# Optimization experiments

Hardware: AMD Instinct MI355X
Metric: run time of the kernel (lower is better)

## Reference

```python
import jax, jax.numpy as jnp
import numpy as np
import math

D_MODEL = 512
N_HEADS = 8
D_K = D_MODEL // N_HEADS
N_SAMPLES = 16
BETA = 1.0
SCALE = 1.0 / math.sqrt(D_K)
PROPOSAL_TEMP = 0.5


def setup_inputs() -> dict:
    key = jax.random.key(0)
    ks = jax.random.split(key, 9)
    B, S = 2, 512
    x = jax.random.normal(ks[0], (B, S, D_MODEL), dtype=jnp.float32)
    init = lambda k: jax.random.normal(k, (D_MODEL, D_MODEL), dtype=jnp.float32) * 0.02
    return {
        "x": x,
        "Wq": init(ks[1]), "bq": jnp.zeros((D_MODEL,), jnp.float32),
        "Wk": init(ks[2]), "bk": jnp.zeros((D_MODEL,), jnp.float32),
        "Wv": init(ks[3]), "bv": jnp.zeros((D_MODEL,), jnp.float32),
        "Wo": init(ks[4]), "bo": jnp.zeros((D_MODEL,), jnp.float32),
    }


def _importance_sampled_weights(scores):
    # scores: [B,H,S,S]. Replicates the per-row Python loop, fully vectorized.
    B, H, Sq, Sk = scores.shape
    target = jax.nn.softmax(scores * BETA, axis=-1)            # [B,H,Sq,Sk]
    # optimal proposal: 0.5*target + 0.5*uniform
    prop = PROPOSAL_TEMP * target + (1.0 - PROPOSAL_TEMP) / Sk
    R = B * H * Sq
    tf = target.reshape(R, Sk)
    pf = prop.reshape(R, Sk)
    # tsu_backend.sample_binary_layer(log(p/(1-p))) == Bernoulli(p) sampling
    s = jax.random.bernoulli(jax.random.key(42), pf[:, None, :], (R, N_SAMPLES, Sk))
    # importance weight = prod(target[sel]) / (prod(prop[sel]) * prod(1-prop[~sel]))
    pt = jnp.prod(jnp.where(s, tf[:, None, :], 1.0), axis=-1)                 # [R,N]
    pp = jnp.prod(jnp.where(s, pf[:, None, :], 1.0 - pf[:, None, :]), axis=-1)
    valid = (s.sum(-1) > 0) & (pp > 0)
    w = jnp.where(valid, pt / jnp.maximum(pp, 1e-38), 0.0)
    ws = w.sum(-1, keepdims=True)
    w = jnp.where(ws > 0, w / jnp.maximum(ws, 1e-38), 1.0 / N_SAMPLES)        # [R,N]
    wa = jnp.einsum('rn,rnk->rk', w, s.astype(jnp.float32))                   # [R,Sk]
    was = wa.sum(-1, keepdims=True)
    wa = jnp.where(was > 0, wa / jnp.maximum(was, 1e-38), 1.0 / Sk)
    return wa.reshape(B, H, Sq, Sk)


def reference(x, Wq, bq, Wk, bk, Wv, bv, Wo, bo):
    B, S, Dm = x.shape
    proj = lambda W, b: (x @ W + b).reshape(B, S, N_HEADS, D_K).transpose(0, 2, 1, 3)
    Q = proj(Wq, bq)  # [B,H,S,dk]
    K = proj(Wk, bk)
    V = proj(Wv, bv)
    scores = jnp.einsum('bhqd,bhkd->bhqk', Q, K) * SCALE
    # torch builds weights via torch.tensor(...) which detaches => constant w.r.t. params
    attn = jax.lax.stop_gradient(_importance_sampled_weights(scores))
    out = jnp.einsum('bhqk,bhkd->bhqd', attn, V)
    out = out.transpose(0, 2, 1, 3).reshape(B, S, Dm)
    return out @ Wo + bo
```

## Files before the change

### kernel.cpp

```cpp
#include <hip/hip_runtime.h>
#include <cstdint>
#include <cstddef>


#define ROTL(x, r) __builtin_rotateleft32((x), (r))

#define QR8(s)                                                                \
  x0[0]+=x1[0];x0[1]+=x1[1];x0[2]+=x1[2];x0[3]+=x1[3];                        \
  x0[4]+=x1[4];x0[5]+=x1[5];x0[6]+=x1[6];x0[7]+=x1[7];                        \
  x1[0]=ROTL(x1[0],s);x1[1]=ROTL(x1[1],s);x1[2]=ROTL(x1[2],s);                \
  x1[3]=ROTL(x1[3],s);x1[4]=ROTL(x1[4],s);x1[5]=ROTL(x1[5],s);                \
  x1[6]=ROTL(x1[6],s);x1[7]=ROTL(x1[7],s);                                    \
  x1[0]^=x0[0];x1[1]^=x0[1];x1[2]^=x0[2];x1[3]^=x0[3];                        \
  x1[4]^=x0[4];x1[5]^=x0[5];x1[6]^=x0[6];x1[7]^=x0[7];
#define INJ8(X, Y)                                                            \
  x0[0]+=(X);x0[1]+=(X);x0[2]+=(X);x0[3]+=(X);                                \
  x0[4]+=(X);x0[5]+=(X);x0[6]+=(X);x0[7]+=(X);                                \
  x1[0]+=(Y);x1[1]+=(Y);x1[2]+=(Y);x1[3]+=(Y);                                \
  x1[4]+=(Y);x1[5]+=(Y);x1[6]+=(Y);x1[7]+=(Y);
#define INJ8Y(Y)                                                              \
  x1[0]+=(Y);x1[1]+=(Y);x1[2]+=(Y);x1[3]+=(Y);                                \
  x1[4]+=(Y);x1[5]+=(Y);x1[6]+=(Y);x1[7]+=(Y);

__global__ __launch_bounds__(256)
void qkv_gemm(const float* __restrict__ x,
              const float* __restrict__ Wq, const float* __restrict__ bq,
              const float* __restrict__ Wk, const float* __restrict__ bk,
              const float* __restrict__ Wv, const float* __restrict__ bv,
              const float* __restrict__ bo, float* __restrict__ outp,
              float* __restrict__ Qw, float* __restrict__ KTw,
              float* __restrict__ Vw) {
  const int tid = threadIdx.x;
  if (blockIdx.z == 3) {
    const int blk = blockIdx.y * 16 + blockIdx.x;
    const size_t base4 = (size_t)blk * 1024 + tid;
    const float4* bo4 = (const float4*)bo;
    float4* out4 = (float4*)outp;
#pragma unroll
    for (int i = 0; i < 4; ++i) {
      const size_t idx4 = base4 + (size_t)i * 256;
      out4[idx4] = bo4[idx4 & 127];
    }
    return;
  }
  const float* W; const float* bias;
  if (blockIdx.z == 0)      { W = Wq; bias = bq; }
  else if (blockIdx.z == 1) { W = Wk; bias = bk; }
  else                      { W = Wv; bias = bv; }

  __shared__ __align__(16) float smem[64 * 68];
  float (*At)[68] = (float(*)[68])smem;
  float (*Bs)[64] = (float(*)[64])(smem + 32 * 68);
  float (*T2)[68] = (float(*)[68])smem;

  const int tx = tid & 15, ty = tid >> 4;
  const int row0 = blockIdx.x * 64, col0 = blockIdx.y * 64;
  float acc[4][4] = {};

  for (int kk = 0; kk < 512; kk += 32) {
    const int ar = tid >> 2;
#pragma unroll
    for (int i = 0; i < 2; ++i) {
      const int kc = ((tid & 3) << 3) + (i << 2);
      const float4 a4 =
          *(const float4*)&x[(size_t)(row0 + ar) * 512 + kk + kc];
      At[kc + 0][ar] = a4.x; At[kc + 1][ar] = a4.y;
      At[kc + 2][ar] = a4.z; At[kc + 3][ar] = a4.w;
    }
#pragma unroll
    for (int i = 0; i < 2; ++i) {
      const int idx = tid + (i << 8);
      const int br = idx >> 4, bc = (idx & 15) << 2;
      *(float4*)&Bs[br][bc] =
          *(const float4*)&W[(size_t)(kk + br) * 512 + col0 + bc];
    }
    __syncthreads();
#pragma unroll
    for (int p = 0; p < 32; ++p) {
      const float4 a4 = *(const float4*)&At[p][ty << 2];
      const float4 b4 = *(const float4*)&Bs[p][tx << 2];
      acc[0][0] = fmaf(a4.x, b4.x, acc[0][0]); acc[0][1] = fmaf(a4.x, b4.y, acc[0][1]);
      acc[0][2] = fmaf(a4.x, b4.z, acc[0][2]); acc[0][3] = fmaf(a4.x, b4.w, acc[0][3]);
      acc[1][0] = fmaf(a4.y, b4.x, acc[1][0]); acc[1][1] = fmaf(a4.y, b4.y, acc[1][1]);
      acc[1][2] = fmaf(a4.y, b4.z, acc[1][2]); acc[1][3] = fmaf(a4.y, b4.w, acc[1][3]);
      acc[2][0] = fmaf(a4.z, b4.x, acc[2][0]); acc[2][1] = fmaf(a4.z, b4.y, acc[2][1]);
      acc[2][2] = fmaf(a4.z, b4.z, acc[2][2]); acc[2][3] = fmaf(a4.z, b4.w, acc[2][3]);
      acc[3][0] = fmaf(a4.w, b4.x, acc[3][0]); acc[3][1] = fmaf(a4.w, b4.y, acc[3][1]);
      acc[3][2] = fmaf(a4.w, b4.z, acc[3][2]); acc[3][3] = fmaf(a4.w, b4.w, acc[3][3]);
    }
    __syncthreads();
  }

  if (blockIdx.z == 0) {
#pragma unroll
    for (int i = 0; i < 4; ++i) {
      const int row = row0 + (ty << 2) + i;
      const int b = row >> 9, s = row & 511;
#pragma unroll
      for (int j = 0; j < 4; ++j) {
        const int col = col0 + (tx << 2) + j;
        const int h = col >> 6, d = col & 63;
        Qw[(((size_t)(b * 8 + h) * 512 + s) * 64) + d] = acc[i][j] + bias[col];
      }
    }
  } else if (blockIdx.z == 1) {
#pragma unroll
    for (int i = 0; i < 4; ++i) {
#pragma unroll
      for (int j = 0; j < 4; ++j) {
        const int col = col0 + (tx << 2) + j;
        T2[(tx << 2) + j][(ty << 2) + i] = acc[i][j] + bias[col];
      }
    }
    __syncthreads();
    const int c = tid >> 2, seg = tid & 3;
    const int b = row0 >> 9, h = blockIdx.y;
    const int s0 = (row0 & 511) + (seg << 4);
    float* dst = KTw + (((size_t)(b * 8 + h) * 64 + c) << 9) + s0;
#pragma unroll
    for (int i2 = 0; i2 < 4; ++i2) {
      *(float4*)&dst[i2 << 2] = *(const float4*)&T2[c][(seg << 4) + (i2 << 2)];
    }
  } else {
#pragma unroll
    for (int i = 0; i < 4; ++i) {
      const int row = row0 + (ty << 2) + i;
      const int b = row >> 9, s = row & 511;
#pragma unroll
      for (int j = 0; j < 4; ++j) {
        const int col = col0 + (tx << 2) + j;
        const int h = col >> 6, d = col & 63;
        Vw[(((size_t)(b * 8 + h) * 512 + s) * 64) + d] = acc[i][j] + bias[col];
      }
    }
  }
}

__global__ __launch_bounds__(256)
void fused_sample(const float* __restrict__ Q, const float* __restrict__ KT,
                  const float* __restrict__ V, const float* __restrict__ Wo,
                  float* __restrict__ outp) {
  const int r = ((blockIdx.x & 7) << 10) + (blockIdx.x >> 3);
  const int bh = r >> 9, q = r & 511;
  const int b = r >> 12, h = (r >> 9) & 7;
  const int tid = threadIdx.x;
  __shared__ __align__(16) float qs[64];
  __shared__ float red[8];
  __shared__ float tf[512];
  __shared__ __align__(16) uint32_t pscu2[512];
  __shared__ float wa[512];
  __shared__ float wr[16];
  __shared__ float redc[8];
  __shared__ float psum[4][64];
  __shared__ float o_s[64];
  __shared__ int   list[512];
  __shared__ int   cnt;

  if (tid == 0) cnt = 0;
  if (tid < 64) qs[tid] = Q[((size_t)bh * 512 + q) * 64 + tid];
  __syncthreads();

  float sc[2];
#pragma unroll
  for (int ii = 0; ii < 2; ++ii) {
    const int k = tid + (ii << 8);
    const float* Kp = KT + (size_t)bh * 64 * 512 + k;
    float s = 0.f;
#pragma unroll
    for (int d4 = 0; d4 < 16; ++d4) {
      const float4 qv = ((const float4*)qs)[d4];
      const float k0 = Kp[(size_t)(d4 * 4 + 0) * 512];
      const float k1 = Kp[(size_t)(d4 * 4 + 1) * 512];
      const float k2 = Kp[(size_t)(d4 * 4 + 2) * 512];
      const float k3 = Kp[(size_t)(d4 * 4 + 3) * 512];
      s = fmaf(qv.x, k0, s); s = fmaf(qv.y, k1, s);
      s = fmaf(qv.z, k2, s); s = fmaf(qv.w, k3, s);
    }
    sc[ii] = s * 0.125f;
  }
  float mx = fmaxf(sc[0], sc[1]);
  for (int m = 1; m < 64; m <<= 1) mx = fmaxf(mx, __shfl_xor(mx, m));
  if ((tid & 63) == 0) red[tid >> 6] = mx;
  __syncthreads();
  const float rowmax = fmaxf(fmaxf(red[0], red[1]), fmaxf(red[2], red[3]));
  const float e0 = expf(sc[0] - rowmax);
  const float e1 = expf(sc[1] - rowmax);
  float ssum = e0 + e1;
  for (int m = 1; m < 64; m <<= 1) ssum += __shfl_xor(ssum, m);
  if ((tid & 63) == 0) red[4 + (tid >> 6)] = ssum;
  __syncthreads();
  const float tot = red[4] + red[5] + red[6] + red[7];
  const float t0 = e0 / tot, t1 = e1 / tot;
  tf[tid] = t0; tf[tid + 256] = t1;
  wa[tid] = 0.f; wa[tid + 256] = 0.f;
  {
    const float p0 = fmaf(0.5f, t0, 0.0009765625f);
    const float p1 = fmaf(0.5f, t1, 0.0009765625f);
    {
      const int k = tid;
      pscu2[(((k & 31) >> 2) << 6) + ((k >> 5) << 2) + (k & 3)] =
          ((uint32_t)ceilf(p0 * 8388608.0f)) << 9;
    }
    {
      const int k = tid + 256;
      pscu2[(((k & 31) >> 2) << 6) + ((k >> 5) << 2) + (k & 3)] =
          ((uint32_t)ceilf(p1 * 8388608.0f)) << 9;
    }
    float ql = (1.f - p0) * (1.f - p1);
    for (int m = 1; m < 64; m <<= 1) ql *= __shfl_xor(ql, m);
    if ((tid & 63) == 0) redc[4 + (tid >> 6)] = ql;
  }
  __syncthreads();
  const float Qrow = redc[4] * redc[5] * redc[6] * redc[7];

  const int n = tid >> 4, t = tid & 15;
  const int k0i = t << 5;
  const uint32_t cbase =
      (uint32_t)r * 8192u + (uint32_t)n * 512u + (uint32_t)k0i + 42u;
  uint32_t bits = 0u;
#pragma unroll
  for (int jb = 0; jb < 32; jb += 8) {
    uint32_t x0[8], x1[8];
#pragma unroll
    for (int i = 0; i < 8; ++i) {
      const uint32_t c = cbase + (uint32_t)(jb + i);
      x0[i] = c;
      x1[i] = ROTL(c, 13) ^ c;
    }
    QR8(15) QR8(26) QR8(6)
    INJ8(42u, 0x1BD11BF1u)
    QR8(17) QR8(29) QR8(16) QR8(24)
    INJ8(0x1BD11BF0u, 2u)
    QR8(13) QR8(15) QR8(26) QR8(6)
    INJ8Y(45u)
    QR8(17) QR8(29) QR8(16) QR8(24)
    INJ8(42u, 0x1BD11BF4u)
    QR8(13) QR8(15) QR8(26) QR8(6)
    INJ8(0x1BD11BF0u, 5u)
    const uint4 pA = *(const uint4*)&pscu2[((jb >> 2) << 6) + (t << 2)];
    const uint4 pB = *(const uint4*)&pscu2[(((jb >> 2) + 1) << 6) + (t << 2)];
    bits |= (uint32_t)((x0[0] ^ x1[0]) < pA.x) << (jb + 0);
    bits |= (uint32_t)((x0[1] ^ x1[1]) < pA.y) << (jb + 1);
    bits |= (uint32_t)((x0[2] ^ x1[2]) < pA.z) << (jb + 2);
    bits |= (uint32_t)((x0[3] ^ x1[3]) < pA.w) << (jb + 3);
    bits |= (uint32_t)((x0[4] ^ x1[4]) < pB.x) << (jb + 4);
    bits |= (uint32_t)((x0[5] ^ x1[5]) < pB.y) << (jb + 5);
    bits |= (uint32_t)((x0[6] ^ x1[6]) < pB.z) << (jb + 6);
    bits |= (uint32_t)((x0[7] ^ x1[7]) < pB.w) << (jb + 7);
  }

  float ptl = 1.f, ratl = 1.f;
  int cl = __popc(bits);
  {
    uint32_t bb = bits;
    while (bb) {
      const int j = __builtin_ctz(bb);
      bb &= bb - 1u;
      const float tv = tf[k0i + j];
      const float p = fmaf(0.5f, tv, 0.0009765625f);
      ptl *= tv;
      ratl *= p / (1.f - p);
    }
  }
#pragma unroll
  for (int m = 1; m < 16; m <<= 1) {
    ptl *= __shfl_xor(ptl, m);
    ratl *= __shfl_xor(ratl, m);
    cl += __shfl_xor(cl, m);
  }
  if (t == 0) {
    const float pp = Qrow * ratl;
    wr[n] = (cl > 0 && pp > 0.f) ? (ptl / fmaxf(pp, 1e-38f)) : 0.f;
  }
  __syncthreads();
  float wsum = 0.f;
#pragma unroll
  for (int m2 = 0; m2 < 16; ++m2) wsum += wr[m2];
  const float wn = (wsum > 0.f) ? (wr[n] / fmaxf(wsum, 1e-38f)) : 0.0625f;
  {
    uint32_t bb = bits;
    while (bb) {
      const int j = __builtin_ctz(bb);
      bb &= bb - 1u;
      atomicAdd(&wa[k0i + j], wn);
    }
  }
  __syncthreads();

  float sp = wa[tid] + wa[tid + 256];
  for (int m = 1; m < 64; m <<= 1) sp += __shfl_xor(sp, m);
  if ((tid & 63) == 0) redc[tid >> 6] = sp;
  if (wa[tid] > 0.f)       { const int i = atomicAdd(&cnt, 1); list[i] = tid; }
  if (wa[tid + 256] > 0.f) { const int i = atomicAdd(&cnt, 1); list[i] = tid + 256; }
  __syncthreads();
  const float was = redc[0] + redc[1] + redc[2] + redc[3];
  const int nnz = cnt;

  const int g = tid >> 6, d = tid & 63;
  const float* Vb = V + ((size_t)(b * 8 + h) * 512) * 64;
  float acc = 0.f;
  if (was > 0.f) {
    const float inv = 1.f / fmaxf(was, 1e-38f);
    for (int i = g; i < nnz; i += 4) {
      const int k = list[i];
      acc = fmaf(wa[k] * inv, Vb[(size_t)k * 64 + d], acc);
    }
  } else {
    for (int k = g; k < 512; k += 4) acc += Vb[(size_t)k * 64 + d];
    acc *= 0.001953125f;
  }
  psum[g][d] = acc;
  __syncthreads();
  if (g == 0)
    o_s[d] = psum[0][d] + psum[1][d] + psum[2][d] + psum[3][d];
  __syncthreads();

  {
    const float* Wh = Wo + ((size_t)h * 64) * 512;
    float a0 = 0.f, a1 = 0.f;
#pragma unroll 8
    for (int dd = 0; dd < 64; ++dd) {
      const float ov = o_s[dd];
      a0 = fmaf(ov, Wh[(size_t)dd * 512 + tid], a0);
      a1 = fmaf(ov, Wh[(size_t)dd * 512 + tid + 256], a1);
    }
    float* orow = outp + ((size_t)(b * 512 + q)) * 512;
    atomicAdd(&orow[tid], a0);
    atomicAdd(&orow[tid + 256], a1);
  }
}

extern "C" void kernel_launch(void* const* d_in, const int* in_sizes, int n_in,
                              void* d_out, int out_size, void* d_ws,
                              size_t ws_size, hipStream_t stream) {
  const float* x  = (const float*)d_in[0];
  const float* Wq = (const float*)d_in[1];
  const float* bq = (const float*)d_in[2];
  const float* Wk = (const float*)d_in[3];
  const float* bk = (const float*)d_in[4];
  const float* Wv = (const float*)d_in[5];
  const float* bv = (const float*)d_in[6];
  const float* Wo = (const float*)d_in[7];
  const float* bo = (const float*)d_in[8];
  float* out = (float*)d_out;

  float* ws = (float*)d_ws;
  float* Qw = ws;
  float* KT = ws + 524288;
  float* Vw = ws + 1048576;

  dim3 gq(16, 8, 4);
  qkv_gemm<<<gq, 256, 0, stream>>>(x, Wq, bq, Wk, bk, Wv, bv, bo, out,
                                   Qw, KT, Vw);
  fused_sample<<<8192, 256, 0, stream>>>(Qw, KT, Vw, Wo, out);
}
```

Baseline: 253.0 us.

## Process four query rows per block and register-prefetch QKV GEMM tiles

The sampling kernel now handles four consecutive query rows per block, so each K column load and each Wo load is reused across four rows, and the grid shrinks to a quarter of its former size. Scores for all four rows are computed together up front, and the softmax/sampling stages then loop over the rows in sequence. The QKV GEMM prefetches the next k-tile into registers while the current tile is being computed. The trade-off is fewer blocks in flight, more serialized per-row sync stages inside each block, and more shared memory and registers per block.

```diff
diff --git a/kernel.cpp b/kernel.cpp
--- a/kernel.cpp
+++ b/kernel.cpp
@@ -57,24 +57,35 @@
   const int row0 = blockIdx.x * 64, col0 = blockIdx.y * 64;
   float acc[4][4] = {};
 
+  const int ar = tid >> 2;
+  const int kc0 = (tid & 3) << 3;
+  const int br0 = tid >> 4,         bc0 = (tid & 15) << 2;
+  const int br1 = (tid + 256) >> 4, bc1 = ((tid + 256) & 15) << 2;
+
+  float4 aReg0, aReg1, bReg0, bReg1;
+  {
+    const int kk = 0;
+    aReg0 = *(const float4*)&x[(size_t)(row0 + ar) * 512 + kk + kc0];
+    aReg1 = *(const float4*)&x[(size_t)(row0 + ar) * 512 + kk + kc0 + 4];
+    bReg0 = *(const float4*)&W[(size_t)(kk + br0) * 512 + col0 + bc0];
+    bReg1 = *(const float4*)&W[(size_t)(kk + br1) * 512 + col0 + bc1];
+  }
+
   for (int kk = 0; kk < 512; kk += 32) {
-    const int ar = tid >> 2;
-#pragma unroll
-    for (int i = 0; i < 2; ++i) {
-      const int kc = ((tid & 3) << 3) + (i << 2);
-      const float4 a4 =
-          *(const float4*)&x[(size_t)(row0 + ar) * 512 + kk + kc];
-      At[kc + 0][ar] = a4.x; At[kc + 1][ar] = a4.y;
-      At[kc + 2][ar] = a4.z; At[kc + 3][ar] = a4.w;
-    }
-#pragma unroll
-    for (int i = 0; i < 2; ++i) {
-      const int idx = tid + (i << 8);
-      const int br = idx >> 4, bc = (idx & 15) << 2;
-      *(float4*)&Bs[br][bc] =
-          *(const float4*)&W[(size_t)(kk + br) * 512 + col0 + bc];
-    }
-    __syncthreads();
+    At[kc0 + 0][ar] = aReg0.x; At[kc0 + 1][ar] = aReg0.y;
+    At[kc0 + 2][ar] = aReg0.z; At[kc0 + 3][ar] = aReg0.w;
+    At[kc0 + 4][ar] = aReg1.x; At[kc0 + 5][ar] = aReg1.y;
+    At[kc0 + 6][ar] = aReg1.z; At[kc0 + 7][ar] = aReg1.w;
+    *(float4*)&Bs[br0][bc0] = bReg0;
+    *(float4*)&Bs[br1][bc1] = bReg1;
+    __syncthreads();
+    if (kk < 480) {
+      const int kn = kk + 32;
+      aReg0 = *(const float4*)&x[(size_t)(row0 + ar) * 512 + kn + kc0];
+      aReg1 = *(const float4*)&x[(size_t)(row0 + ar) * 512 + kn + kc0 + 4];
+      bReg0 = *(const float4*)&W[(size_t)(kn + br0) * 512 + col0 + bc0];
+      bReg1 = *(const float4*)&W[(size_t)(kn + br1) * 512 + col0 + bc1];
+    }
 #pragma unroll
     for (int p = 0; p < 32; ++p) {
       const float4 a4 = *(const float4*)&At[p][ty << 2];
@@ -140,193 +151,233 @@
 void fused_sample(const float* __restrict__ Q, const float* __restrict__ KT,
                   const float* __restrict__ V, const float* __restrict__ Wo,
                   float* __restrict__ outp) {
-  const int r = ((blockIdx.x & 7) << 10) + (blockIdx.x >> 3);
-  const int bh = r >> 9, q = r & 511;
-  const int b = r >> 12, h = (r >> 9) & 7;
+  const int bx = blockIdx.x;
+  const int rbase = ((((bx & 7) << 8) | (bx >> 3)) << 2);
+  const int bh = rbase >> 9, q0 = rbase & 511;
+  const int b = rbase >> 12, h = (rbase >> 9) & 7;
   const int tid = threadIdx.x;
-  __shared__ __align__(16) float qs[64];
+
+  __shared__ __align__(16) float qs[4][64];
+  __shared__ __align__(16) float scs[4][512];
   __shared__ float red[8];
+  __shared__ float redc[8];
+  __shared__ float wr[16];
   __shared__ float tf[512];
   __shared__ __align__(16) uint32_t pscu2[512];
   __shared__ float wa[512];
-  __shared__ float wr[16];
-  __shared__ float redc[8];
   __shared__ float psum[4][64];
-  __shared__ float o_s[64];
+  __shared__ __align__(16) float o_s[4][64];
   __shared__ int   list[512];
   __shared__ int   cnt;
 
-  if (tid == 0) cnt = 0;
-  if (tid < 64) qs[tid] = Q[((size_t)bh * 512 + q) * 64 + tid];
+  qs[tid >> 6][tid & 63] =
+      Q[((size_t)bh * 512 + q0 + (tid >> 6)) * 64 + (tid & 63)];
   __syncthreads();
 
-  float sc[2];
-#pragma unroll
-  for (int ii = 0; ii < 2; ++ii) {
-    const int k = tid + (ii << 8);
-    const float* Kp = KT + (size_t)bh * 64 * 512 + k;
-    float s = 0.f;
+  {
+    const float* Kp = KT + (size_t)bh * 64 * 512 + tid;
+    float s00 = 0.f, s01 = 0.f, s10 = 0.f, s11 = 0.f;
+    float s20 = 0.f, s21 = 0.f, s30 = 0.f, s31 = 0.f;
 #pragma unroll
     for (int d4 = 0; d4 < 16; ++d4) {
-      const float4 qv = ((const float4*)qs)[d4];
-      const float k0 = Kp[(size_t)(d4 * 4 + 0) * 512];
-      const float k1 = Kp[(size_t)(d4 * 4 + 1) * 512];
-      const float k2 = Kp[(size_t)(d4 * 4 + 2) * 512];
-      const float k3 = Kp[(size_t)(d4 * 4 + 3) * 512];
-      s = fmaf(qv.x, k0, s); s = fmaf(qv.y, k1, s);
-      s = fmaf(qv.z, k2, s); s = fmaf(qv.w, k3, s);
-    }
-    sc[ii] = s * 0.125f;
-  }
-  float mx = fmaxf(sc[0], sc[1]);
-  for (int m = 1; m < 64; m <<= 1) mx = fmaxf(mx, __shfl_xor(mx, m));
-  if ((tid & 63) == 0) red[tid >> 6] = mx;
-  __syncthreads();
-  const float rowmax = fmaxf(fmaxf(red[0], red[1]), fmaxf(red[2], red[3]));
-  const float e0 = expf(sc[0] - rowmax);
-  const float e1 = expf(sc[1] - rowmax);
-  float ssum = e0 + e1;
-  for (int m = 1; m < 64; m <<= 1) ssum += __shfl_xor(ssum, m);
-  if ((tid & 63) == 0) red[4 + (tid >> 6)] = ssum;
-  __syncthreads();
-  const float tot = red[4] + red[5] + red[6] + red[7];
-  const float t0 = e0 / tot, t1 = e1 / tot;
-  tf[tid] = t0; tf[tid + 256] = t1;
-  wa[tid] = 0.f; wa[tid + 256] = 0.f;
-  {
-    const float p0 = fmaf(0.5f, t0, 0.0009765625f);
-    const float p1 = fmaf(0.5f, t1, 0.0009765625f);
-    {
-      const int k = tid;
-      pscu2[(((k & 31) >> 2) << 6) + ((k >> 5) << 2) + (k & 3)] =
-          ((uint32_t)ceilf(p0 * 8388608.0f)) << 9;
-    }
-    {
-      const int k = tid + 256;
-      pscu2[(((k & 31) >> 2) << 6) + ((k >> 5) << 2) + (k & 3)] =
-          ((uint32_t)ceilf(p1 * 8388608.0f)) << 9;
-    }
-    float ql = (1.f - p0) * (1.f - p1);
-    for (int m = 1; m < 64; m <<= 1) ql *= __shfl_xor(ql, m);
-    if ((tid & 63) == 0) redc[4 + (tid >> 6)] = ql;
-  }
-  __syncthreads();
-  const float Qrow = redc[4] * redc[5] * redc[6] * redc[7];
+      float k0v[4], k1v[4];
+#pragma unroll
+      for (int j = 0; j < 4; ++j) {
+        k0v[j] = Kp[(size_t)(d4 * 4 + j) * 512];
+        k1v[j] = Kp[(size_t)(d4 * 4 + j) * 512 + 256];
+      }
+      const float4 q0v = *(const float4*)&qs[0][d4 << 2];
+      const float4 q1v = *(const float4*)&qs[1][d4 << 2];
+      const float4 q2v = *(const float4*)&qs[2][d4 << 2];
+      const float4 q3v = *(const float4*)&qs[3][d4 << 2];
+      s00 = fmaf(q0v.x, k0v[0], s00); s00 = fmaf(q0v.y, k0v[1], s00);
+      s00 = fmaf(q0v.z, k0v[2], s00); s00 = fmaf(q0v.w, k0v[3], s00);
+      s01 = fmaf(q0v.x, k1v[0], s01); s01 = fmaf(q0v.y, k1v[1], s01);
+      s01 = fmaf(q0v.z, k1v[2], s01); s01 = fmaf(q0v.w, k1v[3], s01);
+      s10 = fmaf(q1v.x, k0v[0], s10); s10 = fmaf(q1v.y, k0v[1], s10);
+      s10 = fmaf(q1v.z, k0v[2], s10); s10 = fmaf(q1v.w, k0v[3], s10);
+      s11 = fmaf(q1v.x, k1v[0], s11); s11 = fmaf(q1v.y, k1v[1], s11);
+      s11 = fmaf(q1v.z, k1v[2], s11); s11 = fmaf(q1v.w, k1v[3], s11);
+      s20 = fmaf(q2v.x, k0v[0], s20); s20 = fmaf(q2v.y, k0v[1], s20);
+      s20 = fmaf(q2v.z, k0v[2], s20); s20 = fmaf(q2v.w, k0v[3], s20);
+      s21 = fmaf(q2v.x, k1v[0], s21); s21 = fmaf(q2v.y, k1v[1], s21);
+      s21 = fmaf(q2v.z, k1v[2], s21); s21 = fmaf(q2v.w, k1v[3], s21);
+      s30 = fmaf(q3v.x, k0v[0], s30); s30 = fmaf(q3v.y, k0v[1], s30);
+      s30 = fmaf(q3v.z, k0v[2], s30); s30 = fmaf(q3v.w, k0v[3], s30);
+      s31 = fmaf(q3v.x, k1v[0], s31); s31 = fmaf(q3v.y, k1v[1], s31);
+      s31 = fmaf(q3v.z, k1v[2], s31); s31 = fmaf(q3v.w, k1v[3], s31);
+    }
+    scs[0][tid] = s00 * 0.125f; scs[0][tid + 256] = s01 * 0.125f;
+    scs[1][tid] = s10 * 0.125f; scs[1][tid + 256] = s11 * 0.125f;
+    scs[2][tid] = s20 * 0.125f; scs[2][tid + 256] = s21 * 0.125f;
+    scs[3][tid] = s30 * 0.125f; scs[3][tid + 256] = s31 * 0.125f;
+  }
 
   const int n = tid >> 4, t = tid & 15;
   const int k0i = t << 5;
-  const uint32_t cbase =
-      (uint32_t)r * 8192u + (uint32_t)n * 512u + (uint32_t)k0i + 42u;
-  uint32_t bits = 0u;
-#pragma unroll
-  for (int jb = 0; jb < 32; jb += 8) {
-    uint32_t x0[8], x1[8];
-#pragma unroll
-    for (int i = 0; i < 8; ++i) {
-      const uint32_t c = cbase + (uint32_t)(jb + i);
-      x0[i] = c;
-      x1[i] = ROTL(c, 13) ^ c;
-    }
-    QR8(15) QR8(26) QR8(6)
-    INJ8(42u, 0x1BD11BF1u)
-    QR8(17) QR8(29) QR8(16) QR8(24)
-    INJ8(0x1BD11BF0u, 2u)
-    QR8(13) QR8(15) QR8(26) QR8(6)
-    INJ8Y(45u)
-    QR8(17) QR8(29) QR8(16) QR8(24)
-    INJ8(42u, 0x1BD11BF4u)
-    QR8(13) QR8(15) QR8(26) QR8(6)
-    INJ8(0x1BD11BF0u, 5u)
-    const uint4 pA = *(const uint4*)&pscu2[((jb >> 2) << 6) + (t << 2)];
-    const uint4 pB = *(const uint4*)&pscu2[(((jb >> 2) + 1) << 6) + (t << 2)];
-    bits |= (uint32_t)((x0[0] ^ x1[0]) < pA.x) << (jb + 0);
-    bits |= (uint32_t)((x0[1] ^ x1[1]) < pA.y) << (jb + 1);
-    bits |= (uint32_t)((x0[2] ^ x1[2]) < pA.z) << (jb + 2);
-    bits |= (uint32_t)((x0[3] ^ x1[3]) < pA.w) << (jb + 3);
-    bits |= (uint32_t)((x0[4] ^ x1[4]) < pB.x) << (jb + 4);
-    bits |= (uint32_t)((x0[5] ^ x1[5]) < pB.y) << (jb + 5);
-    bits |= (uint32_t)((x0[6] ^ x1[6]) < pB.z) << (jb + 6);
-    bits |= (uint32_t)((x0[7] ^ x1[7]) < pB.w) << (jb + 7);
-  }
-
-  float ptl = 1.f, ratl = 1.f;
-  int cl = __popc(bits);
-  {
-    uint32_t bb = bits;
-    while (bb) {
-      const int j = __builtin_ctz(bb);
-      bb &= bb - 1u;
-      const float tv = tf[k0i + j];
-      const float p = fmaf(0.5f, tv, 0.0009765625f);
-      ptl *= tv;
-      ratl *= p / (1.f - p);
-    }
-  }
-#pragma unroll
-  for (int m = 1; m < 16; m <<= 1) {
-    ptl *= __shfl_xor(ptl, m);
-    ratl *= __shfl_xor(ratl, m);
-    cl += __shfl_xor(cl, m);
-  }
-  if (t == 0) {
-    const float pp = Qrow * ratl;
-    wr[n] = (cl > 0 && pp > 0.f) ? (ptl / fmaxf(pp, 1e-38f)) : 0.f;
-  }
-  __syncthreads();
-  float wsum = 0.f;
-#pragma unroll
-  for (int m2 = 0; m2 < 16; ++m2) wsum += wr[m2];
-  const float wn = (wsum > 0.f) ? (wr[n] / fmaxf(wsum, 1e-38f)) : 0.0625f;
-  {
-    uint32_t bb = bits;
-    while (bb) {
-      const int j = __builtin_ctz(bb);
-      bb &= bb - 1u;
-      atomicAdd(&wa[k0i + j], wn);
-    }
-  }
-  __syncthreads();
-
-  float sp = wa[tid] + wa[tid + 256];
-  for (int m = 1; m < 64; m <<= 1) sp += __shfl_xor(sp, m);
-  if ((tid & 63) == 0) redc[tid >> 6] = sp;
-  if (wa[tid] > 0.f)       { const int i = atomicAdd(&cnt, 1); list[i] = tid; }
-  if (wa[tid + 256] > 0.f) { const int i = atomicAdd(&cnt, 1); list[i] = tid + 256; }
-  __syncthreads();
-  const float was = redc[0] + redc[1] + redc[2] + redc[3];
-  const int nnz = cnt;
-
   const int g = tid >> 6, d = tid & 63;
   const float* Vb = V + ((size_t)(b * 8 + h) * 512) * 64;
-  float acc = 0.f;
-  if (was > 0.f) {
-    const float inv = 1.f / fmaxf(was, 1e-38f);
-    for (int i = g; i < nnz; i += 4) {
-      const int k = list[i];
-      acc = fmaf(wa[k] * inv, Vb[(size_t)k * 64 + d], acc);
-    }
-  } else {
-    for (int k = g; k < 512; k += 4) acc += Vb[(size_t)k * 64 + d];
-    acc *= 0.001953125f;
-  }
-  psum[g][d] = acc;
-  __syncthreads();
-  if (g == 0)
-    o_s[d] = psum[0][d] + psum[1][d] + psum[2][d] + psum[3][d];
+
+  for (int rr = 0; rr < 4; ++rr) {
+    const int r = rbase + rr;
+    const float sc0 = scs[rr][tid];
+    const float sc1 = scs[rr][tid + 256];
+
+    float mx = fmaxf(sc0, sc1);
+    for (int m = 1; m < 64; m <<= 1) mx = fmaxf(mx, __shfl_xor(mx, m));
+    if ((tid & 63) == 0) red[tid >> 6] = mx;
+    __syncthreads();
+    const float rowmax = fmaxf(fmaxf(red[0], red[1]), fmaxf(red[2], red[3]));
+    const float e0 = expf(sc0 - rowmax);
+    const float e1 = expf(sc1 - rowmax);
+    float ssum = e0 + e1;
+    for (int m = 1; m < 64; m <<= 1) ssum += __shfl_xor(ssum, m);
+    if ((tid & 63) == 0) red[4 + (tid >> 6)] = ssum;
+    if (tid == 0) cnt = 0;
+    __syncthreads();
+    const float tot = red[4] + red[5] + red[6] + red[7];
+    const float t0 = e0 / tot, t1 = e1 / tot;
+    tf[tid] = t0; tf[tid + 256] = t1;
+    wa[tid] = 0.f; wa[tid + 256] = 0.f;
+    {
+      const float p0 = fmaf(0.5f, t0, 0.0009765625f);
+      const float p1 = fmaf(0.5f, t1, 0.0009765625f);
+      {
+        const int k = tid;
+        pscu2[(((k & 31) >> 2) << 6) + ((k >> 5) << 2) + (k & 3)] =
+            ((uint32_t)ceilf(p0 * 8388608.0f)) << 9;
+      }
+      {
+        const int k = tid + 256;
+        pscu2[(((k & 31) >> 2) << 6) + ((k >> 5) << 2) + (k & 3)] =
+            ((uint32_t)ceilf(p1 * 8388608.0f)) << 9;
+      }
+      float ql = (1.f - p0) * (1.f - p1);
+      for (int m = 1; m < 64; m <<= 1) ql *= __shfl_xor(ql, m);
+      if ((tid & 63) == 0) redc[4 + (tid >> 6)] = ql;
+    }
+    __syncthreads();
+    const float Qrow = redc[4] * redc[5] * redc[6] * redc[7];
+
+    const uint32_t cbase =
+        (uint32_t)r * 8192u + (uint32_t)n * 512u + (uint32_t)k0i + 42u;
+    uint32_t bits = 0u;
+#pragma unroll
+    for (int jb = 0; jb < 32; jb += 8) {
+      uint32_t x0[8], x1[8];
+#pragma unroll
+      for (int i = 0; i < 8; ++i) {
+        const uint32_t c = cbase + (uint32_t)(jb + i);
+        x0[i] = c;
+        x1[i] = ROTL(c, 13) ^ c;
+      }
+      QR8(15) QR8(26) QR8(6)
+      INJ8(42u, 0x1BD11BF1u)
+      QR8(17) QR8(29) QR8(16) QR8(24)
+      INJ8(0x1BD11BF0u, 2u)
+      QR8(13) QR8(15) QR8(26) QR8(6)
+      INJ8Y(45u)
+      QR8(17) QR8(29) QR8(16) QR8(24)
+      INJ8(42u, 0x1BD11BF4u)
+      QR8(13) QR8(15) QR8(26) QR8(6)
+      INJ8(0x1BD11BF0u, 5u)
+      const uint4 pA = *(const uint4*)&pscu2[((jb >> 2) << 6) + (t << 2)];
+      const uint4 pB = *(const uint4*)&pscu2[(((jb >> 2) + 1) << 6) + (t << 2)];
+      bits |= (uint32_t)((x0[0] ^ x1[0]) < pA.x) << (jb + 0);
+      bits |= (uint32_t)((x0[1] ^ x1[1]) < pA.y) << (jb + 1);
+      bits |= (uint32_t)((x0[2] ^ x1[2]) < pA.z) << (jb + 2);
+      bits |= (uint32_t)((x0[3] ^ x1[3]) < pA.w) << (jb + 3);
+      bits |= (uint32_t)((x0[4] ^ x1[4]) < pB.x) << (jb + 4);
+      bits |= (uint32_t)((x0[5] ^ x1[5]) < pB.y) << (jb + 5);
+      bits |= (uint32_t)((x0[6] ^ x1[6]) < pB.z) << (jb + 6);
+      bits |= (uint32_t)((x0[7] ^ x1[7]) < pB.w) << (jb + 7);
+    }
+
+    float ptl = 1.f, ratl = 1.f;
+    int cl = __popc(bits);
+    {
+      uint32_t bb = bits;
+      while (bb) {
+        const int j = __builtin_ctz(bb);
+        bb &= bb - 1u;
+        const float tv = tf[k0i + j];
+        const float p = fmaf(0.5f, tv, 0.0009765625f);
+        ptl *= tv;
+        ratl *= p / (1.f - p);
+      }
+    }
+#pragma unroll
+    for (int m = 1; m < 16; m <<= 1) {
+      ptl *= __shfl_xor(ptl, m);
+      ratl *= __shfl_xor(ratl, m);
+      cl += __shfl_xor(cl, m);
+    }
+    if (t == 0) {
+      const float pp = Qrow * ratl;
+      wr[n] = (cl > 0 && pp > 0.f) ? (ptl / fmaxf(pp, 1e-38f)) : 0.f;
+    }
+    __syncthreads();
+    float wsum = 0.f;
+#pragma unroll
+    for (int m2 = 0; m2 < 16; ++m2) wsum += wr[m2];
+    const float wn = (wsum > 0.f) ? (wr[n] / fmaxf(wsum, 1e-38f)) : 0.0625f;
+    {
+      uint32_t bb = bits;
+      while (bb) {
+        const int j = __builtin_ctz(bb);
+        bb &= bb - 1u;
+        atomicAdd(&wa[k0i + j], wn);
+      }
+    }
+    __syncthreads();
+
+    float sp = wa[tid] + wa[tid + 256];
+    for (int m = 1; m < 64; m <<= 1) sp += __shfl_xor(sp, m);
+    if ((tid & 63) == 0) redc[tid >> 6] = sp;
+    if (wa[tid] > 0.f)       { const int i = atomicAdd(&cnt, 1); list[i] = tid; }
+    if (wa[tid + 256] > 0.f) { const int i = atomicAdd(&cnt, 1); list[i] = tid + 256; }
+    __syncthreads();
+    const float was = redc[0] + redc[1] + redc[2] + redc[3];
+    const int nnz = cnt;
+
+    float acc = 0.f;
+    if (was > 0.f) {
+      const float inv = 1.f / fmaxf(was, 1e-38f);
+      for (int i = g; i < nnz; i += 4) {
+        const int k = list[i];
+        acc = fmaf(wa[k] * inv, Vb[(size_t)k * 64 + d], acc);
+      }
+    } else {
+      for (int k = g; k < 512; k += 4) acc += Vb[(size_t)k * 64 + d];
+      acc *= 0.001953125f;
+    }
+    psum[g][d] = acc;
+    __syncthreads();
+    if (g == 0)
+      o_s[rr][d] = psum[0][d] + psum[1][d] + psum[2][d] + psum[3][d];
+  }
   __syncthreads();
 
   {
     const float* Wh = Wo + ((size_t)h * 64) * 512;
-    float a0 = 0.f, a1 = 0.f;
+    float a00 = 0.f, a01 = 0.f, a10 = 0.f, a11 = 0.f;
+    float a20 = 0.f, a21 = 0.f, a30 = 0.f, a31 = 0.f;
 #pragma unroll 8
     for (int dd = 0; dd < 64; ++dd) {
-      const float ov = o_s[dd];
-      a0 = fmaf(ov, Wh[(size_t)dd * 512 + tid], a0);
-      a1 = fmaf(ov, Wh[(size_t)dd * 512 + tid + 256], a1);
-    }
-    float* orow = outp + ((size_t)(b * 512 + q)) * 512;
-    atomicAdd(&orow[tid], a0);
-    atomicAdd(&orow[tid + 256], a1);
+      const float w0 = Wh[(size_t)dd * 512 + tid];
+      const float w1 = Wh[(size_t)dd * 512 + tid + 256];
+      const float o0 = o_s[0][dd], o1 = o_s[1][dd];
+      const float o2 = o_s[2][dd], o3 = o_s[3][dd];
+      a00 = fmaf(o0, w0, a00); a01 = fmaf(o0, w1, a01);
+      a10 = fmaf(o1, w0, a10); a11 = fmaf(o1, w1, a11);
+      a20 = fmaf(o2, w0, a20); a21 = fmaf(o2, w1, a21);
+      a30 = fmaf(o3, w0, a30); a31 = fmaf(o3, w1, a31);
+    }
+    float* orow = outp + ((size_t)(b * 512 + q0)) * 512;
+    atomicAdd(&orow[tid], a00);         atomicAdd(&orow[tid + 256], a01);
+    atomicAdd(&orow[512 + tid], a10);   atomicAdd(&orow[512 + tid + 256], a11);
+    atomicAdd(&orow[1024 + tid], a20);  atomicAdd(&orow[1024 + tid + 256], a21);
+    atomicAdd(&orow[1536 + tid], a30);  atomicAdd(&orow[1536 + tid + 256], a31);
   }
 }
 
@@ -352,5 +403,5 @@
   dim3 gq(16, 8, 4);
   qkv_gemm<<<gq, 256, 0, stream>>>(x, Wq, bq, Wk, bk, Wv, bv, bo, out,
                                    Qw, KT, Vw);
-  fused_sample<<<8192, 256, 0, stream>>>(Qw, KT, Vw, Wo, out);
+  fused_sample<<<2048, 256, 0, stream>>>(Qw, KT, Vw, Wo, out);
 }
```

Result: faster. 247.8 us (-2.1%).
